# Performance work log

Measured on AMD Instinct MI355X. Metric: run time of the kernel, lower is better.

Reference implementation:

```python
import jax, jax.numpy as jnp
import numpy as np

H, HKV, DH = 16, 8, 128
G = H // HKV
EPS = 1e-6
ROPE_THETA = 1000000.0


def _rms_norm(x, w):
    # RMSNorm over last dim (head_dim)
    var = jnp.mean(x * x, axis=-1, keepdims=True)
    return x * jax.lax.rsqrt(var + EPS) * w


def _rotate_half(x):
    x1, x2 = jnp.split(x, 2, axis=-1)
    return jnp.concatenate([-x2, x1], axis=-1)


def setup_inputs() -> dict:
    key = jax.random.key(0)
    ks = jax.random.split(key, 5)
    B, T, D = 2, 2048, 2048
    s = 0.02
    return {
        "x": jax.random.normal(ks[0], (B, T, D), jnp.float32),
        "wq": jax.random.normal(ks[1], (H * DH, D), jnp.float32) * s,
        "wk": jax.random.normal(ks[2], (HKV * DH, D), jnp.float32) * s,
        "wv": jax.random.normal(ks[3], (HKV * DH, D), jnp.float32) * s,
        "wo": jax.random.normal(ks[4], (D, H * DH), jnp.float32) * s,
        "q_norm_w": jnp.ones((DH,), jnp.float32),
        "k_norm_w": jnp.ones((DH,), jnp.float32),
    }


def reference(x, wq, wk, wv, wo, q_norm_w, k_norm_w):
    B, T, D = x.shape
    # projections (nn.Linear: y = x @ W^T)
    q = (x @ wq.T).reshape(B, T, H, DH).transpose(0, 2, 1, 3)      # [B,H,T,Dh]
    k = (x @ wk.T).reshape(B, T, HKV, DH).transpose(0, 2, 1, 3)    # [B,Hkv,T,Dh]
    v = (x @ wv.T).reshape(B, T, HKV, DH).transpose(0, 2, 1, 3)    # [B,Hkv,T,Dh]

    # QK RMSNorm
    q = _rms_norm(q, q_norm_w)
    k = _rms_norm(k, k_norm_w)

    # RoPE (half-split style), positions 0..T-1
    inv_freq = 1.0 / (ROPE_THETA ** (jnp.arange(0, DH, 2, dtype=jnp.float32) / DH))
    freqs = jnp.arange(T, dtype=jnp.float32)[:, None] * inv_freq[None, :]   # [T,Dh/2]
    emb = jnp.concatenate([freqs, freqs], axis=-1)                           # [T,Dh]
    cos = jnp.cos(emb)[None, None, :, :]
    sin = jnp.sin(emb)[None, None, :, :]
    q = q * cos + _rotate_half(q) * sin
    k = k * cos + _rotate_half(k) * sin

    # GQA attention with fp32 scores and causal mask
    qg = q.reshape(B, HKV, G, T, DH)
    scores = jnp.einsum("bhgtd,bhkd->bhgtk", qg.astype(jnp.float32),
                        k.astype(jnp.float32)) / jnp.sqrt(jnp.float32(DH))
    causal = jnp.tril(jnp.ones((T, T), dtype=bool))[None, None, None, :, :]
    scores = jnp.where(causal, scores, jnp.finfo(jnp.float32).min)
    attn = jax.nn.softmax(scores, axis=-1).astype(x.dtype)
    ctx = jnp.einsum("bhgtk,bhkd->bhgtd", attn, v)                            # [B,Hkv,G,T,Dh]
    out = ctx.reshape(B, H, T, DH).transpose(0, 2, 1, 3).reshape(B, T, H * DH)
    return out @ wo.T
```

## Files before the change

kernel.cpp:

```cpp
#include <hip/hip_runtime.h>
#include <cstdint>

#define Hq 16
#define HKVn 8
#define DHn 128
#define Tn 2048
#define Bn 2
#define Dm 2048
#define BT (Bn*Tn)

typedef __attribute__((ext_vector_type(8))) short bfrag8;
typedef __attribute__((ext_vector_type(4))) float facc4;
typedef __attribute__((ext_vector_type(4))) _Float16 f16x4;
typedef __attribute__((ext_vector_type(8))) _Float16 f16x8;
typedef __attribute__((ext_vector_type(8))) unsigned short us8;

__device__ __forceinline__ unsigned short f2bf(float f) {
    union { float f; unsigned int u; } v; v.f = f;
    unsigned int u = v.u;
    unsigned int r = (u + 0x7FFFu + ((u >> 16) & 1u)) >> 16;
    return (unsigned short)r;
}
__device__ __forceinline__ float bf2f(unsigned short u) {
    union { unsigned int u; float f; } v; v.u = ((unsigned int)u) << 16;
    return v.f;
}

__global__ __launch_bounds__(256) void cvt_all(const float* __restrict__ x,
                                               const float* __restrict__ wq,
                                               const float* __restrict__ wk,
                                               const float* __restrict__ wv,
                                               const float* __restrict__ wo,
                                               unsigned short* __restrict__ x_bf,
                                               unsigned short* __restrict__ wqkv_bf,
                                               unsigned short* __restrict__ wo_bf,
                                               float* __restrict__ lut) {
    int i = blockIdx.x * 256 + threadIdx.x;
    if (i >= 5242880) {
        int ii = i - 5242880;
        int t = ii >> 6, d = ii & 63;
        float fr = exp2f(-(float)d * 0.3114307588956902f);
        float ang = (float)t * fr;
        float sv, cv;
        __sincosf(ang, &sv, &cv);
        lut[t * 128 + d] = cv;
        lut[t * 128 + 64 + d] = sv;
        return;
    }
    const float4* src; ushort4* dst;
    if (i < 2097152)      { src = (const float4*)x  + i;            dst = (ushort4*)x_bf + i; }
    else if (i < 3145728) { src = (const float4*)wq + (i-2097152);  dst = (ushort4*)wqkv_bf + (i-2097152); }
    else if (i < 3670016) { src = (const float4*)wk + (i-3145728);  dst = (ushort4*)wqkv_bf + 1048576 + (i-3145728); }
    else if (i < 4194304) { src = (const float4*)wv + (i-3670016);  dst = (ushort4*)wqkv_bf + 1572864 + (i-3670016); }
    else                  { src = (const float4*)wo + (i-4194304);  dst = (ushort4*)wo_bf + (i-4194304); }
    float4 v = *src;
    ushort4 y;
    y.x = f2bf(v.x); y.y = f2bf(v.y); y.z = f2bf(v.z); y.w = f2bf(v.w);
    *dst = y;
}

__device__ __forceinline__ size_t koff_tiled(int t, int d) {
    int kc = (t >> 4) & 3, l15 = t & 15;
    int f = d >> 5, qd = (d >> 3) & 3, j = d & 7;
    return (size_t)(t >> 6) * 8192 + ((((kc * 4 + f) * 64 + qd * 16 + l15) << 3) + j);
}

__device__ __forceinline__ void stage_half(const unsigned short* __restrict__ g0,
                                           int rowBase, int k0, char* region, int h, int tid) {
#pragma unroll
    for (int s = 0; s < 2; s++) {
        int c = h * 1024 + s * 512 + tid;
        int r = c >> 3;
        int kk = (c & 7) ^ (r & 7);
        const unsigned short* g = g0 + (size_t)(rowBase + r) * 2048 + k0 + kk * 8;
        __builtin_amdgcn_global_load_lds((const __attribute__((address_space(1))) void*)g,
            (__attribute__((address_space(3))) void*)(region + c * 16), 16, 0, 0);
    }
}

__device__ __forceinline__ void stage_half_bt(const unsigned short* __restrict__ g0,
                                              int rowBase, int k0, char* region, int h,
                                              int tid, int K) {
#pragma unroll
    for (int s = 0; s < 2; s++) {
        int c = h * 512 + s * 256 + tid;
        int r = c >> 3;
        int kk = (c & 7) ^ (r & 7);
        const unsigned short* g = g0 + (size_t)(rowBase + r) * K + k0 + kk * 8;
        __builtin_amdgcn_global_load_lds((const __attribute__((address_space(1))) void*)g,
            (__attribute__((address_space(3))) void*)(region + c * 16), 16, 0, 0);
    }
}

__global__ __launch_bounds__(256, 2) void gemm_bt(const unsigned short* __restrict__ A,
                                                  const unsigned short* __restrict__ Bm,
                                                  float* __restrict__ C,
                                                  int M, int N, int K) {
    __shared__ char smem[65536];
    int nt = K >> 6;
    int tid = threadIdx.x;
    int w = tid >> 6, lane = tid & 63, quad = lane >> 4, l15 = lane & 15;
    int wr = w >> 1, wc = w & 1;
    int rowBase = blockIdx.y * 128, colBase = blockIdx.x * 128;
    facc4 acc[4][4];
#pragma unroll
    for (int i = 0; i < 4; i++)
#pragma unroll
        for (int j = 0; j < 4; j++) acc[i][j] = facc4{0.f, 0.f, 0.f, 0.f};

    char* b0A = smem;          char* b0B = smem + 16384;
    char* b1A = smem + 32768;  char* b1B = smem + 49152;
    stage_half_bt(A,  rowBase, 0,  b0A, 0, tid, K);
    stage_half_bt(A,  rowBase, 0,  b0A, 1, tid, K);
    stage_half_bt(Bm, colBase, 0,  b0B, 0, tid, K);
    stage_half_bt(Bm, colBase, 0,  b0B, 1, tid, K);
    stage_half_bt(Bm, colBase, 64, b1B, 0, tid, K);
    stage_half_bt(A,  rowBase, 64, b1A, 0, tid, K);
    stage_half_bt(A,  rowBase, 64, b1A, 1, tid, K);
    asm volatile("s_waitcnt vmcnt(6)" ::: "memory");
    __builtin_amdgcn_s_barrier();

    bfrag8 a01[2][2], a23[2][2], b01[2][2], b23[2][2];
#pragma unroll
    for (int m = 0; m < 2; m++)
#pragma unroll
        for (int kh = 0; kh < 2; kh++) {
            int row = wr * 64 + m * 16 + l15;
            int ch = (kh * 4 + quad) ^ (row & 7);
            a01[m][kh] = *(const bfrag8*)(b0A + row * 128 + ch * 16);
        }
#pragma unroll
    for (int n = 0; n < 2; n++)
#pragma unroll
        for (int kh = 0; kh < 2; kh++) {
            int row = wc * 64 + n * 16 + l15;
            int ch = (kh * 4 + quad) ^ (row & 7);
            b01[n][kh] = *(const bfrag8*)(b0B + row * 128 + ch * 16);
        }

#pragma unroll 1
    for (int t = 0; t < nt; t++) {
        __builtin_amdgcn_sched_barrier(0);
        char* bA = smem + (t & 1) * 32768;
        char* bB = bA + 16384;
        char* oA = smem + ((t & 1) ^ 1) * 32768;
        char* oB = oA + 16384;
        int k1 = (t + 1) * 64, k2 = (t + 2) * 64;

#pragma unroll
        for (int n = 0; n < 2; n++)
#pragma unroll
            for (int kh = 0; kh < 2; kh++) {
                int row = wc * 64 + (2 + n) * 16 + l15;
                int ch = (kh * 4 + quad) ^ (row & 7);
                b23[n][kh] = *(const bfrag8*)(bB + row * 128 + ch * 16);
            }
        if (t + 1 < nt) stage_half_bt(Bm, colBase, k1, oB, 1, tid, K);
        __builtin_amdgcn_sched_barrier(0);
        __builtin_amdgcn_s_barrier();
        __builtin_amdgcn_s_setprio(1);
#pragma unroll
        for (int m = 0; m < 2; m++)
#pragma unroll
            for (int n = 0; n < 2; n++)
#pragma unroll
                for (int kh = 0; kh < 2; kh++)
                    acc[m][n] = __builtin_amdgcn_mfma_f32_16x16x32_bf16(a01[m][kh], b01[n][kh], acc[m][n], 0, 0, 0);
        __builtin_amdgcn_s_setprio(0);
        __builtin_amdgcn_s_barrier();

#pragma unroll
        for (int m = 0; m < 2; m++)
#pragma unroll
            for (int kh = 0; kh < 2; kh++) {
                int row = wr * 64 + (2 + m) * 16 + l15;
                int ch = (kh * 4 + quad) ^ (row & 7);
                a23[m][kh] = *(const bfrag8*)(bA + row * 128 + ch * 16);
            }
        __builtin_amdgcn_sched_barrier(0);
        __builtin_amdgcn_s_barrier();
        __builtin_amdgcn_s_setprio(1);
#pragma unroll
        for (int m = 0; m < 2; m++)
#pragma unroll
            for (int n = 0; n < 2; n++)
#pragma unroll
                for (int kh = 0; kh < 2; kh++)
                    acc[m][2 + n] = __builtin_amdgcn_mfma_f32_16x16x32_bf16(a01[m][kh], b23[n][kh], acc[m][2 + n], 0, 0, 0);
        __builtin_amdgcn_s_setprio(0);
        __builtin_amdgcn_s_barrier();

        if (t + 2 < nt) stage_half_bt(Bm, colBase, k2, bB, 0, tid, K);
        __builtin_amdgcn_sched_barrier(0);
        __builtin_amdgcn_s_barrier();
        __builtin_amdgcn_s_setprio(1);
#pragma unroll
        for (int m = 0; m < 2; m++)
#pragma unroll
            for (int n = 0; n < 2; n++)
#pragma unroll
                for (int kh = 0; kh < 2; kh++)
                    acc[2 + m][2 + n] = __builtin_amdgcn_mfma_f32_16x16x32_bf16(a23[m][kh], b23[n][kh], acc[2 + m][2 + n], 0, 0, 0);
        __builtin_amdgcn_s_setprio(0);
        __builtin_amdgcn_s_barrier();

        if (t + 2 < nt) {
            stage_half_bt(A, rowBase, k2, bA, 0, tid, K);
            stage_half_bt(A, rowBase, k2, bA, 1, tid, K);
            asm volatile("s_waitcnt vmcnt(6)" ::: "memory");
        } else if (t + 1 < nt) {
            asm volatile("s_waitcnt vmcnt(0)" ::: "memory");
        }
        __builtin_amdgcn_sched_barrier(0);
        __builtin_amdgcn_s_barrier();
        __builtin_amdgcn_s_setprio(1);
#pragma unroll
        for (int m = 0; m < 2; m++)
#pragma unroll
            for (int n = 0; n < 2; n++)
#pragma unroll
                for (int kh = 0; kh < 2; kh++)
                    acc[2 + m][n] = __builtin_amdgcn_mfma_f32_16x16x32_bf16(a23[m][kh], b01[n][kh], acc[2 + m][n], 0, 0, 0);
        __builtin_amdgcn_s_setprio(0);
        if (t + 1 < nt) {
#pragma unroll
            for (int m = 0; m < 2; m++)
#pragma unroll
                for (int kh = 0; kh < 2; kh++) {
                    int row = wr * 64 + m * 16 + l15;
                    int ch = (kh * 4 + quad) ^ (row & 7);
                    a01[m][kh] = *(const bfrag8*)(oA + row * 128 + ch * 16);
                }
#pragma unroll
            for (int n = 0; n < 2; n++)
#pragma unroll
                for (int kh = 0; kh < 2; kh++) {
                    int row = wc * 64 + n * 16 + l15;
                    int ch = (kh * 4 + quad) ^ (row & 7);
                    b01[n][kh] = *(const bfrag8*)(oB + row * 128 + ch * 16);
                }
        }
        __builtin_amdgcn_s_barrier();
    }

#pragma unroll
    for (int i = 0; i < 4; i++)
#pragma unroll
        for (int j = 0; j < 4; j++)
#pragma unroll
            for (int r = 0; r < 4; r++) {
                int row = rowBase + wr * 64 + i * 16 + quad * 4 + r;
                int col = colBase + wc * 64 + j * 16 + l15;
                C[(size_t)row * N + col] = acc[i][j][r];
            }
}

__global__ __launch_bounds__(512, 2) void gemm_qkv_fused(const unsigned short* __restrict__ A,
                                                         const unsigned short* __restrict__ Bm,
                                                         const float* __restrict__ qw,
                                                         const float* __restrict__ kw,
                                                         const float* __restrict__ lut,
                                                         unsigned short* __restrict__ q_bf,
                                                         unsigned short* __restrict__ k_bf,
                                                         _Float16* __restrict__ vT) {
    __shared__ char smem[131072];
    const int NT = 32;
    int tid = threadIdx.x;
    int w = tid >> 6, lane = tid & 63, quad = lane >> 4, l15 = lane & 15;
    int wr = w >> 2, wc = w & 3;
    int u = ((blockIdx.x & 7) << 5) | (blockIdx.x >> 3);
    int bx = u & 15, by = u >> 4;
    int rowBase = by * 256, colBase = bx * 256;

    facc4 acc[8][4];
#pragma unroll
    for (int m = 0; m < 8; m++)
#pragma unroll
        for (int n = 0; n < 4; n++) acc[m][n] = facc4{0.f, 0.f, 0.f, 0.f};

    char* b0A = smem;           char* b0B = smem + 32768;
    char* b1A = smem + 65536;   char* b1B = smem + 98304;
    stage_half(A,  rowBase, 0,  b0A, 0, tid);
    stage_half(A,  rowBase, 0,  b0A, 1, tid);
    stage_half(Bm, colBase, 0,  b0B, 0, tid);
    stage_half(Bm, colBase, 0,  b0B, 1, tid);
    stage_half(Bm, colBase, 64, b1B, 0, tid);
    stage_half(A,  rowBase, 64, b1A, 0, tid);
    stage_half(A,  rowBase, 64, b1A, 1, tid);
    asm volatile("s_waitcnt vmcnt(6)" ::: "memory");
    __builtin_amdgcn_s_barrier();

    bfrag8 a03[4][2], a47[4][2], b01[2][2], b23[2][2];
#pragma unroll
    for (int m = 0; m < 4; m++)
#pragma unroll
        for (int kh = 0; kh < 2; kh++) {
            int row = wr * 128 + m * 16 + l15;
            int ch = (kh * 4 + quad) ^ (row & 7);
            a03[m][kh] = *(const bfrag8*)(b0A + row * 128 + ch * 16);
        }
#pragma unroll
    for (int n = 0; n < 2; n++)
#pragma unroll
        for (int kh = 0; kh < 2; kh++) {
            int row = wc * 64 + n * 16 + l15;
            int ch = (kh * 4 + quad) ^ (row & 7);
            b01[n][kh] = *(const bfrag8*)(b0B + row * 128 + ch * 16);
        }

#pragma unroll 1
    for (int t = 0; t < NT; t++) {
        __builtin_amdgcn_sched_barrier(0);
        char* bA = smem + (t & 1) * 65536;
        char* bB = bA + 32768;
        char* oA = smem + ((t & 1) ^ 1) * 65536;
        char* oB = oA + 32768;
        int k1 = (t + 1) * 64, k2 = (t + 2) * 64;

#pragma unroll
        for (int n = 0; n < 2; n++)
#pragma unroll
            for (int kh = 0; kh < 2; kh++) {
                int row = wc * 64 + (2 + n) * 16 + l15;
                int ch = (kh * 4 + quad) ^ (row & 7);
                b23[n][kh] = *(const bfrag8*)(bB + row * 128 + ch * 16);
            }
        if (t + 1 < NT) stage_half(Bm, colBase, k1, oB, 1, tid);
        __builtin_amdgcn_sched_barrier(0);
        __builtin_amdgcn_s_barrier();
        __builtin_amdgcn_s_setprio(1);
#pragma unroll
        for (int m = 0; m < 4; m++)
#pragma unroll
            for (int n = 0; n < 2; n++)
#pragma unroll
                for (int kh = 0; kh < 2; kh++)
                    acc[m][n] = __builtin_amdgcn_mfma_f32_16x16x32_bf16(a03[m][kh], b01[n][kh], acc[m][n], 0, 0, 0);
        __builtin_amdgcn_s_setprio(0);
        __builtin_amdgcn_s_barrier();

#pragma unroll
        for (int m = 0; m < 4; m++)
#pragma unroll
            for (int kh = 0; kh < 2; kh++) {
                int row = wr * 128 + (4 + m) * 16 + l15;
                int ch = (kh * 4 + quad) ^ (row & 7);
                a47[m][kh] = *(const bfrag8*)(bA + row * 128 + ch * 16);
            }
        __builtin_amdgcn_sched_barrier(0);
        __builtin_amdgcn_s_barrier();
        __builtin_amdgcn_s_setprio(1);
#pragma unroll
        for (int m = 0; m < 4; m++)
#pragma unroll
            for (int n = 0; n < 2; n++)
#pragma unroll
                for (int kh = 0; kh < 2; kh++)
                    acc[m][2 + n] = __builtin_amdgcn_mfma_f32_16x16x32_bf16(a03[m][kh], b23[n][kh], acc[m][2 + n], 0, 0, 0);
        __builtin_amdgcn_s_setprio(0);
        __builtin_amdgcn_s_barrier();

        if (t + 2 < NT) stage_half(Bm, colBase, k2, bB, 0, tid);
        __builtin_amdgcn_sched_barrier(0);
        __builtin_amdgcn_s_barrier();
        __builtin_amdgcn_s_setprio(1);
#pragma unroll
        for (int m = 0; m < 4; m++)
#pragma unroll
            for (int n = 0; n < 2; n++)
#pragma unroll
                for (int kh = 0; kh < 2; kh++)
                    acc[4 + m][2 + n] = __builtin_amdgcn_mfma_f32_16x16x32_bf16(a47[m][kh], b23[n][kh], acc[4 + m][2 + n], 0, 0, 0);
        __builtin_amdgcn_s_setprio(0);
        __builtin_amdgcn_s_barrier();

        if (t + 2 < NT) {
            stage_half(A, rowBase, k2, bA, 0, tid);
            stage_half(A, rowBase, k2, bA, 1, tid);
            asm volatile("s_waitcnt vmcnt(6)" ::: "memory");
        } else if (t + 1 < NT) {
            asm volatile("s_waitcnt vmcnt(0)" ::: "memory");
        }
        __builtin_amdgcn_sched_barrier(0);
        __builtin_amdgcn_s_barrier();
        __builtin_amdgcn_s_setprio(1);
#pragma unroll
        for (int m = 0; m < 4; m++)
#pragma unroll
            for (int n = 0; n < 2; n++)
#pragma unroll
                for (int kh = 0; kh < 2; kh++)
                    acc[4 + m][n] = __builtin_amdgcn_mfma_f32_16x16x32_bf16(a47[m][kh], b01[n][kh], acc[4 + m][n], 0, 0, 0);
        __builtin_amdgcn_s_setprio(0);
        if (t + 1 < NT) {
#pragma unroll
            for (int m = 0; m < 4; m++)
#pragma unroll
                for (int kh = 0; kh < 2; kh++) {
                    int row = wr * 128 + m * 16 + l15;
                    int ch = (kh * 4 + quad) ^ (row & 7);
                    a03[m][kh] = *(const bfrag8*)(oA + row * 128 + ch * 16);
                }
#pragma unroll
            for (int n = 0; n < 2; n++)
#pragma unroll
                for (int kh = 0; kh < 2; kh++) {
                    int row = wc * 64 + n * 16 + l15;
                    int ch = (kh * 4 + quad) ^ (row & 7);
                    b01[n][kh] = *(const bfrag8*)(oB + row * 128 + ch * 16);
                }
        }
        __builtin_amdgcn_s_barrier();
    }

    if (bx >= 12) {
        int hv = (bx - 12) * 2 + (wc >> 1);
#pragma unroll
        for (int half = 0; half < 2; half++) {
            int gt0 = rowBase + wr * 128 + half * 64;
            int bb = gt0 >> 11, t64 = (gt0 & 2047) >> 6;
            _Float16* vbase = vT + ((size_t)(bb * 8 + hv) * 32 + t64) * 8192;
#pragma unroll
            for (int mm = 0; mm < 4; mm++) {
                int kcp = mm >> 1, hh = mm & 1;
#pragma unroll
                for (int n = 0; n < 4; n++) {
                    int dblk = (wc & 1) * 4 + n;
                    f16x4 pv;
#pragma unroll
                    for (int r = 0; r < 4; r++) pv[r] = (_Float16)acc[half * 4 + mm][n][r];
                    *(f16x4*)(vbase + (((dblk * 2 + kcp) * 64 + quad * 16 + l15) * 8) + hh * 4) = pv;
                }
            }
        }
        return;
    }

    const float* wn = (bx < 8) ? qw : kw;
    const float osc = (bx < 8) ? (0.08838834764831845f * 1.4426950408889634f) : 1.0f;
    float* sums = (float*)smem;
#pragma unroll
    for (int m = 0; m < 8; m++)
#pragma unroll
        for (int r = 0; r < 4; r++) {
            float s = 0.f;
#pragma unroll
            for (int n = 0; n < 4; n++) s += acc[m][n][r] * acc[m][n][r];
            s += __shfl_xor(s, 1); s += __shfl_xor(s, 2);
            s += __shfl_xor(s, 4); s += __shfl_xor(s, 8);
            if (l15 == 0) sums[wc * 256 + wr * 128 + m * 16 + quad * 4 + r] = s;
        }
    __syncthreads();
    int hw = wc >> 1;
    float inv[8][4];
#pragma unroll
    for (int m = 0; m < 8; m++)
#pragma unroll
        for (int r = 0; r < 4; r++) {
            int row = wr * 128 + m * 16 + quad * 4 + r;
            float tot = sums[(2 * hw) * 256 + row] + sums[(2 * hw + 1) * 256 + row];
            inv[m][r] = rsqrtf(tot * (1.0f / 128.0f) + 1e-6f);
        }
    __syncthreads();
    unsigned short* tileb = (unsigned short*)(smem + hw * 65536);
    float wcol[4];
#pragma unroll
    for (int n = 0; n < 4; n++) wcol[n] = wn[(wc & 1) * 64 + n * 16 + l15];
#pragma unroll
    for (int m = 0; m < 8; m++)
#pragma unroll
        for (int r = 0; r < 4; r++) {
            int row = wr * 128 + m * 16 + quad * 4 + r;
            int sw = (row & 7) << 4;
#pragma unroll
            for (int n = 0; n < 4; n++) {
                int cb = ((wc & 1) * 64 + n * 16 + l15) * 2;
                *(unsigned short*)((char*)tileb + row * 256 + (cb ^ sw)) =
                    f2bf(acc[m][n][r] * inv[m][r] * wcol[n]);
            }
        }
    __syncthreads();
    {
        int row = tid >> 1, d0 = (tid & 1) * 32;
        int gt = rowBase + row;
        int tt = gt & 2047, bb = gt >> 11;
        const float* lc = lut + tt * 128;
        int sw = (row & 7) << 4;
#pragma unroll
        for (int hh2 = 0; hh2 < 2; hh2++) {
            const char* tb = (const char*)(smem + hh2 * 65536);
            unsigned short* qrow = 0; unsigned short* kplane = 0;
            if (bx < 8) qrow = q_bf + ((size_t)(bb * 16 + bx * 2 + hh2) * 2048 + tt) * 128;
            else        kplane = k_bf + (size_t)(bb * 8 + (bx - 8) * 2 + hh2) * 2048 * 128;
#pragma unroll
            for (int dc = 0; dc < 32; dc += 8) {
                int db = d0 + dc;
                us8 n0u = *(const us8*)(tb + row * 256 + ((2 * db) ^ sw));
                us8 n1u = *(const us8*)(tb + row * 256 + ((2 * db + 128) ^ sw));
                float4 cA = *(const float4*)(lc + db), cB = *(const float4*)(lc + db + 4);
                float4 sA = *(const float4*)(lc + 64 + db), sB = *(const float4*)(lc + 64 + db + 4);
                float cv[8] = {cA.x, cA.y, cA.z, cA.w, cB.x, cB.y, cB.z, cB.w};
                float sv[8] = {sA.x, sA.y, sA.z, sA.w, sB.x, sB.y, sB.z, sB.w};
                us8 p0, p1;
#pragma unroll
                for (int e = 0; e < 8; e++) {
                    float a0 = bf2f(n0u[e]), a1 = bf2f(n1u[e]);
                    p0[e] = f2bf((a0 * cv[e] - a1 * sv[e]) * osc);
                    p1[e] = f2bf((a1 * cv[e] + a0 * sv[e]) * osc);
                }
                if (bx < 8) {
                    *(us8*)(qrow + db) = p0;
                    *(us8*)(qrow + db + 64) = p1;
                } else {
                    *(us8*)(kplane + koff_tiled(tt, db)) = p0;
                    *(us8*)(kplane + koff_tiled(tt, db + 64)) = p1;
                }
            }
        }
    }
}

__global__ __launch_bounds__(256, 2) void attn_kernel(const unsigned short* __restrict__ q_bf,
                                                      const unsigned short* __restrict__ k_glob,
                                                      const _Float16* __restrict__ v_glob,
                                                      unsigned short* __restrict__ ctx) {
    __shared__ char smem[65536];
    int tid = threadIdx.x;
    int w = tid >> 6, lane = tid & 63, quad = lane >> 4, l15 = lane & 15;
    int bid = blockIdx.x;
    int u = bid & 255, halfg = bid >> 8;
    int j = u & 7, h = (u >> 3) & 15, b = (u >> 7) & 1;
    int qblk = halfg ? j : 15 - j;
    int hkv = h >> 1;
    int qb = qblk * 128;
    int qw0 = qb + w * 32;

    const unsigned short* qp = q_bf + (size_t)(b * Hq + h) * Tn * 128;
    const unsigned short* ktile = k_glob + (size_t)(b * HKVn + hkv) * 32 * 8192;
    const _Float16* vtile = v_glob + (size_t)(b * HKVn + hkv) * 32 * 8192;

    bfrag8 qf[2][4];
#pragma unroll
    for (int g = 0; g < 2; g++) {
        int row = qw0 + g * 16 + l15;
#pragma unroll
        for (int f = 0; f < 4; f++)
            qf[g][f] = *(const bfrag8*)(qp + (size_t)row * 128 + f * 32 + quad * 8);
    }

    facc4 o0[8], o1[8];
#pragma unroll
    for (int jj = 0; jj < 8; jj++) { o0[jj] = facc4{0.f,0.f,0.f,0.f}; o1[jj] = facc4{0.f,0.f,0.f,0.f}; }
    float m0 = -__builtin_inff(), m1 = -__builtin_inff(), l0 = 0.f, l1 = 0.f;

    int nkb = qb / 64 + 2;
#pragma unroll
    for (int i = 0; i < 4; i++) {
        const unsigned short* gk = ktile + (size_t)(i * 256 + tid) * 8;
        __builtin_amdgcn_global_load_lds((const __attribute__((address_space(1))) void*)gk,
            (__attribute__((address_space(3))) void*)(smem + i * 4096 + w * 1024), 16, 0, 0);
        const _Float16* gv = vtile + (size_t)(i * 256 + tid) * 8;
        __builtin_amdgcn_global_load_lds((const __attribute__((address_space(1))) void*)gv,
            (__attribute__((address_space(3))) void*)(smem + 16384 + i * 4096 + w * 1024), 16, 0, 0);
    }

    for (int ib = 0; ib < nkb; ib++) {
        int kb = ib * 64;
        __syncthreads();
        if (ib + 1 < nkb) {
            char* nb = smem + ((ib + 1) & 1) * 32768;
#pragma unroll
            for (int i = 0; i < 4; i++) {
                const unsigned short* gk = ktile + (size_t)(ib + 1) * 8192 + (i * 256 + tid) * 8;
                __builtin_amdgcn_global_load_lds((const __attribute__((address_space(1))) void*)gk,
                    (__attribute__((address_space(3))) void*)(nb + i * 4096 + w * 1024), 16, 0, 0);
                const _Float16* gv = vtile + (size_t)(ib + 1) * 8192 + (i * 256 + tid) * 8;
                __builtin_amdgcn_global_load_lds((const __attribute__((address_space(1))) void*)gv,
                    (__attribute__((address_space(3))) void*)(nb + 16384 + i * 4096 + w * 1024), 16, 0, 0);
            }
        }
        char* cb = smem + (ib & 1) * 32768;
        if (kb <= qw0 + 31) {
            facc4 s0[4], s1[4];
#pragma unroll
            for (int kc = 0; kc < 4; kc++) {
                bfrag8 kf[4];
#pragma unroll
                for (int f = 0; f < 4; f++)
                    kf[f] = *(const bfrag8*)(cb + (((kc * 4 + f) * 64 + lane) << 4));
                facc4 a = facc4{0.f,0.f,0.f,0.f}, bq = facc4{0.f,0.f,0.f,0.f};
#pragma unroll
                for (int f = 0; f < 4; f++) {
                    a  = __builtin_amdgcn_mfma_f32_16x16x32_bf16(kf[f], qf[0][f], a, 0, 0, 0);
                    bq = __builtin_amdgcn_mfma_f32_16x16x32_bf16(kf[f], qf[1][f], bq, 0, 0, 0);
                }
                s0[kc] = a; s1[kc] = bq;
            }
            if (kb + 63 > qw0) {
                int q0 = qw0 + l15, q1 = q0 + 16;
#pragma unroll
                for (int kc = 0; kc < 4; kc++)
#pragma unroll
                    for (int r = 0; r < 4; r++) {
                        int k = kb + kc * 16 + quad * 4 + r;
                        if (k > q0) s0[kc][r] = -__builtin_inff();
                        if (k > q1) s1[kc][r] = -__builtin_inff();
                    }
            }
            float mx0 = s0[0][0], mx1 = s1[0][0];
#pragma unroll
            for (int kc = 0; kc < 4; kc++)
#pragma unroll
                for (int r = 0; r < 4; r++) {
                    mx0 = fmaxf(mx0, s0[kc][r]); mx1 = fmaxf(mx1, s1[kc][r]);
                }
            mx0 = fmaxf(mx0, __shfl_xor(mx0, 16)); mx0 = fmaxf(mx0, __shfl_xor(mx0, 32));
            mx1 = fmaxf(mx1, __shfl_xor(mx1, 16)); mx1 = fmaxf(mx1, __shfl_xor(mx1, 32));
            if (!__all((mx0 - m0 <= 8.f) && (mx1 - m1 <= 8.f))) {
                float mn0 = fmaxf(m0, mx0), mn1 = fmaxf(m1, mx1);
                float alpha0 = exp2f(m0 - mn0), alpha1 = exp2f(m1 - mn1);
                m0 = mn0; m1 = mn1;
                l0 *= alpha0; l1 *= alpha1;
#pragma unroll
                for (int jj = 0; jj < 8; jj++)
#pragma unroll
                    for (int r = 0; r < 4; r++) { o0[jj][r] *= alpha0; o1[jj][r] *= alpha1; }
            }
            float rs0 = 0.f, rs1 = 0.f;
#pragma unroll
            for (int kc = 0; kc < 4; kc++)
#pragma unroll
                for (int r = 0; r < 4; r++) {
                    s0[kc][r] = exp2f(s0[kc][r] - m0); rs0 += s0[kc][r];
                    s1[kc][r] = exp2f(s1[kc][r] - m1); rs1 += s1[kc][r];
                }
            rs0 += __shfl_xor(rs0, 16); rs0 += __shfl_xor(rs0, 32);
            rs1 += __shfl_xor(rs1, 16); rs1 += __shfl_xor(rs1, 32);
            l0 += rs0; l1 += rs1;
            f16x4 pb0[4], pb1[4];
#pragma unroll
            for (int kc = 0; kc < 4; kc++) {
                pb0[kc] = f16x4{(_Float16)s0[kc][0], (_Float16)s0[kc][1],
                                (_Float16)s0[kc][2], (_Float16)s0[kc][3]};
                pb1[kc] = f16x4{(_Float16)s1[kc][0], (_Float16)s1[kc][1],
                                (_Float16)s1[kc][2], (_Float16)s1[kc][3]};
            }
#pragma unroll
            for (int kcp = 0; kcp < 2; kcp++)
#pragma unroll
                for (int dblk = 0; dblk < 8; dblk++) {
                    f16x8 vv = *(const f16x8*)(cb + 16384 + (((dblk * 2 + kcp) * 64 + lane) << 4));
                    f16x4 a0 = f16x4{vv[0], vv[1], vv[2], vv[3]};
                    f16x4 a1 = f16x4{vv[4], vv[5], vv[6], vv[7]};
                    o0[dblk] = __builtin_amdgcn_mfma_f32_16x16x16f16(a0, pb0[kcp*2],   o0[dblk], 0, 0, 0);
                    o0[dblk] = __builtin_amdgcn_mfma_f32_16x16x16f16(a1, pb0[kcp*2+1], o0[dblk], 0, 0, 0);
                    o1[dblk] = __builtin_amdgcn_mfma_f32_16x16x16f16(a0, pb1[kcp*2],   o1[dblk], 0, 0, 0);
                    o1[dblk] = __builtin_amdgcn_mfma_f32_16x16x16f16(a1, pb1[kcp*2+1], o1[dblk], 0, 0, 0);
                }
        }
    }
    float inv0 = 1.0f / l0, inv1 = 1.0f / l1;
#pragma unroll
    for (int g = 0; g < 2; g++) {
        int q = qw0 + g * 16 + l15;
        float invl = g ? inv1 : inv0;
#pragma unroll
        for (int dblk = 0; dblk < 8; dblk++) {
            facc4 ov = g ? o1[dblk] : o0[dblk];
            ushort4 st;
            st.x = f2bf(ov[0] * invl); st.y = f2bf(ov[1] * invl);
            st.z = f2bf(ov[2] * invl); st.w = f2bf(ov[3] * invl);
            *(ushort4*)(ctx + ((size_t)(b * Tn + q)) * 2048 + h * 128 + dblk * 16 + quad * 4) = st;
        }
    }
}

extern "C" void kernel_launch(void* const* d_in, const int* in_sizes, int n_in,
                              void* d_out, int out_size, void* d_ws, size_t ws_size,
                              hipStream_t stream) {
    (void)in_sizes; (void)n_in; (void)out_size; (void)ws_size;
    const float* x  = (const float*)d_in[0];
    const float* wq = (const float*)d_in[1];
    const float* wk = (const float*)d_in[2];
    const float* wv = (const float*)d_in[3];
    const float* wo = (const float*)d_in[4];
    const float* qw = (const float*)d_in[5];
    const float* kw = (const float*)d_in[6];
    float* out = (float*)d_out;
    char* ws = (char*)d_ws;

    unsigned short* x_bf    = (unsigned short*)(ws);
    unsigned short* wqkv_bf = (unsigned short*)(ws + 16777216);
    unsigned short* wo_bf   = (unsigned short*)(ws + 33554432);
    unsigned short* q_bf    = (unsigned short*)(ws + 41943040);
    unsigned short* k_bf    = (unsigned short*)(ws + 58720256);
    _Float16*       vT_f16  = (_Float16*)(ws + 67108864);
    unsigned short* ctx_bf  = (unsigned short*)(ws + 75497472);
    float*          lut     = (float*)(ws + 92274688);

    cvt_all<<<20992, 256, 0, stream>>>(x, wq, wk, wv, wo, x_bf, wqkv_bf, wo_bf, lut);
    gemm_qkv_fused<<<256, 512, 0, stream>>>(x_bf, wqkv_bf, qw, kw, lut, q_bf, k_bf, vT_f16);
    attn_kernel<<<512, 256, 0, stream>>>(q_bf, k_bf, vT_f16, ctx_bf);
    gemm_bt<<<dim3(16, 32), 256, 0, stream>>>(ctx_bf, wo_bf, out, 4096, 2048, 2048);
}
```

Measured before the change: 313.0 us.

## Shrink attention query tile to 64 rows and read V directly from global

The attention kernel now gives each block 64 query rows (16 per wave) instead of 128, doubling the grid to 1024 blocks and raising the occupancy hint to 4 blocks per CU. V tiles are no longer staged in LDS; each wave reads its V fragments straight from global memory, so LDS use halves and only K is double-buffered. This aims for more parallelism and better causal load balance. The cost is that K/V reuse per block falls and V traffic goes through uncached-in-LDS global loads on the critical path.

```diff
diff --git a/kernel.cpp b/kernel.cpp
--- a/kernel.cpp
+++ b/kernel.cpp
@@ -520,158 +520,134 @@
     }
 }
 
-__global__ __launch_bounds__(256, 2) void attn_kernel(const unsigned short* __restrict__ q_bf,
+__global__ __launch_bounds__(256, 4) void attn_kernel(const unsigned short* __restrict__ q_bf,
                                                       const unsigned short* __restrict__ k_glob,
                                                       const _Float16* __restrict__ v_glob,
                                                       unsigned short* __restrict__ ctx) {
-    __shared__ char smem[65536];
+    __shared__ char smem[32768];
     int tid = threadIdx.x;
     int w = tid >> 6, lane = tid & 63, quad = lane >> 4, l15 = lane & 15;
     int bid = blockIdx.x;
-    int u = bid & 255, halfg = bid >> 8;
-    int j = u & 7, h = (u >> 3) & 15, b = (u >> 7) & 1;
-    int qblk = halfg ? j : 15 - j;
+    int u = bid & 511, halfg = bid >> 9;
+    int j = u & 15, h = (u >> 4) & 15, b = (u >> 8) & 1;
+    int qblk = halfg ? j : 31 - j;
     int hkv = h >> 1;
-    int qb = qblk * 128;
-    int qw0 = qb + w * 32;
+    int qb = qblk * 64;
+    int qw0 = qb + w * 16;
 
     const unsigned short* qp = q_bf + (size_t)(b * Hq + h) * Tn * 128;
     const unsigned short* ktile = k_glob + (size_t)(b * HKVn + hkv) * 32 * 8192;
     const _Float16* vtile = v_glob + (size_t)(b * HKVn + hkv) * 32 * 8192;
 
-    bfrag8 qf[2][4];
-#pragma unroll
-    for (int g = 0; g < 2; g++) {
-        int row = qw0 + g * 16 + l15;
+    bfrag8 qf[4];
+    {
+        int row = qw0 + l15;
 #pragma unroll
         for (int f = 0; f < 4; f++)
-            qf[g][f] = *(const bfrag8*)(qp + (size_t)row * 128 + f * 32 + quad * 8);
-    }
-
-    facc4 o0[8], o1[8];
-#pragma unroll
-    for (int jj = 0; jj < 8; jj++) { o0[jj] = facc4{0.f,0.f,0.f,0.f}; o1[jj] = facc4{0.f,0.f,0.f,0.f}; }
-    float m0 = -__builtin_inff(), m1 = -__builtin_inff(), l0 = 0.f, l1 = 0.f;
-
-    int nkb = qb / 64 + 2;
+            qf[f] = *(const bfrag8*)(qp + (size_t)row * 128 + f * 32 + quad * 8);
+    }
+
+    facc4 o[8];
+#pragma unroll
+    for (int d = 0; d < 8; d++) o[d] = facc4{0.f, 0.f, 0.f, 0.f};
+    float m0 = -__builtin_inff(), l0 = 0.f;
+
+    int nkb = qblk + 1;
 #pragma unroll
     for (int i = 0; i < 4; i++) {
         const unsigned short* gk = ktile + (size_t)(i * 256 + tid) * 8;
         __builtin_amdgcn_global_load_lds((const __attribute__((address_space(1))) void*)gk,
             (__attribute__((address_space(3))) void*)(smem + i * 4096 + w * 1024), 16, 0, 0);
-        const _Float16* gv = vtile + (size_t)(i * 256 + tid) * 8;
-        __builtin_amdgcn_global_load_lds((const __attribute__((address_space(1))) void*)gv,
-            (__attribute__((address_space(3))) void*)(smem + 16384 + i * 4096 + w * 1024), 16, 0, 0);
     }
 
     for (int ib = 0; ib < nkb; ib++) {
         int kb = ib * 64;
         __syncthreads();
         if (ib + 1 < nkb) {
-            char* nb = smem + ((ib + 1) & 1) * 32768;
+            char* nb = smem + ((ib + 1) & 1) * 16384;
 #pragma unroll
             for (int i = 0; i < 4; i++) {
                 const unsigned short* gk = ktile + (size_t)(ib + 1) * 8192 + (i * 256 + tid) * 8;
                 __builtin_amdgcn_global_load_lds((const __attribute__((address_space(1))) void*)gk,
                     (__attribute__((address_space(3))) void*)(nb + i * 4096 + w * 1024), 16, 0, 0);
-                const _Float16* gv = vtile + (size_t)(ib + 1) * 8192 + (i * 256 + tid) * 8;
-                __builtin_amdgcn_global_load_lds((const __attribute__((address_space(1))) void*)gv,
-                    (__attribute__((address_space(3))) void*)(nb + 16384 + i * 4096 + w * 1024), 16, 0, 0);
-            }
-        }
-        char* cb = smem + (ib & 1) * 32768;
-        if (kb <= qw0 + 31) {
-            facc4 s0[4], s1[4];
+            }
+        }
+        char* cb = smem + (ib & 1) * 16384;
+        if (kb <= qw0 + 15) {
+            facc4 s0[4];
 #pragma unroll
             for (int kc = 0; kc < 4; kc++) {
                 bfrag8 kf[4];
 #pragma unroll
                 for (int f = 0; f < 4; f++)
                     kf[f] = *(const bfrag8*)(cb + (((kc * 4 + f) * 64 + lane) << 4));
-                facc4 a = facc4{0.f,0.f,0.f,0.f}, bq = facc4{0.f,0.f,0.f,0.f};
-#pragma unroll
-                for (int f = 0; f < 4; f++) {
-                    a  = __builtin_amdgcn_mfma_f32_16x16x32_bf16(kf[f], qf[0][f], a, 0, 0, 0);
-                    bq = __builtin_amdgcn_mfma_f32_16x16x32_bf16(kf[f], qf[1][f], bq, 0, 0, 0);
-                }
-                s0[kc] = a; s1[kc] = bq;
+                facc4 a = facc4{0.f, 0.f, 0.f, 0.f};
+#pragma unroll
+                for (int f = 0; f < 4; f++)
+                    a = __builtin_amdgcn_mfma_f32_16x16x32_bf16(kf[f], qf[f], a, 0, 0, 0);
+                s0[kc] = a;
             }
             if (kb + 63 > qw0) {
-                int q0 = qw0 + l15, q1 = q0 + 16;
+                int q0 = qw0 + l15;
 #pragma unroll
                 for (int kc = 0; kc < 4; kc++)
 #pragma unroll
                     for (int r = 0; r < 4; r++) {
                         int k = kb + kc * 16 + quad * 4 + r;
                         if (k > q0) s0[kc][r] = -__builtin_inff();
-                        if (k > q1) s1[kc][r] = -__builtin_inff();
                     }
             }
-            float mx0 = s0[0][0], mx1 = s1[0][0];
+            float mx0 = s0[0][0];
 #pragma unroll
             for (int kc = 0; kc < 4; kc++)
 #pragma unroll
-                for (int r = 0; r < 4; r++) {
-                    mx0 = fmaxf(mx0, s0[kc][r]); mx1 = fmaxf(mx1, s1[kc][r]);
-                }
+                for (int r = 0; r < 4; r++) mx0 = fmaxf(mx0, s0[kc][r]);
             mx0 = fmaxf(mx0, __shfl_xor(mx0, 16)); mx0 = fmaxf(mx0, __shfl_xor(mx0, 32));
-            mx1 = fmaxf(mx1, __shfl_xor(mx1, 16)); mx1 = fmaxf(mx1, __shfl_xor(mx1, 32));
-            if (!__all((mx0 - m0 <= 8.f) && (mx1 - m1 <= 8.f))) {
-                float mn0 = fmaxf(m0, mx0), mn1 = fmaxf(m1, mx1);
-                float alpha0 = exp2f(m0 - mn0), alpha1 = exp2f(m1 - mn1);
-                m0 = mn0; m1 = mn1;
-                l0 *= alpha0; l1 *= alpha1;
-#pragma unroll
-                for (int jj = 0; jj < 8; jj++)
-#pragma unroll
-                    for (int r = 0; r < 4; r++) { o0[jj][r] *= alpha0; o1[jj][r] *= alpha1; }
-            }
-            float rs0 = 0.f, rs1 = 0.f;
+            if (!__all(mx0 - m0 <= 8.f)) {
+                float mn0 = fmaxf(m0, mx0);
+                float alpha0 = exp2f(m0 - mn0);
+                m0 = mn0;
+                l0 *= alpha0;
+#pragma unroll
+                for (int d = 0; d < 8; d++)
+#pragma unroll
+                    for (int r = 0; r < 4; r++) o[d][r] *= alpha0;
+            }
+            float rs0 = 0.f;
 #pragma unroll
             for (int kc = 0; kc < 4; kc++)
 #pragma unroll
                 for (int r = 0; r < 4; r++) {
                     s0[kc][r] = exp2f(s0[kc][r] - m0); rs0 += s0[kc][r];
-                    s1[kc][r] = exp2f(s1[kc][r] - m1); rs1 += s1[kc][r];
                 }
             rs0 += __shfl_xor(rs0, 16); rs0 += __shfl_xor(rs0, 32);
-            rs1 += __shfl_xor(rs1, 16); rs1 += __shfl_xor(rs1, 32);
-            l0 += rs0; l1 += rs1;
-            f16x4 pb0[4], pb1[4];
-#pragma unroll
-            for (int kc = 0; kc < 4; kc++) {
-                pb0[kc] = f16x4{(_Float16)s0[kc][0], (_Float16)s0[kc][1],
-                                (_Float16)s0[kc][2], (_Float16)s0[kc][3]};
-                pb1[kc] = f16x4{(_Float16)s1[kc][0], (_Float16)s1[kc][1],
-                                (_Float16)s1[kc][2], (_Float16)s1[kc][3]};
-            }
+            l0 += rs0;
+            f16x4 pb[4];
+#pragma unroll
+            for (int kc = 0; kc < 4; kc++)
+                pb[kc] = f16x4{(_Float16)s0[kc][0], (_Float16)s0[kc][1],
+                               (_Float16)s0[kc][2], (_Float16)s0[kc][3]};
+            const _Float16* vb = vtile + (size_t)ib * 8192;
 #pragma unroll
             for (int kcp = 0; kcp < 2; kcp++)
 #pragma unroll
                 for (int dblk = 0; dblk < 8; dblk++) {
-                    f16x8 vv = *(const f16x8*)(cb + 16384 + (((dblk * 2 + kcp) * 64 + lane) << 4));
+                    f16x8 vv = *(const f16x8*)(vb + (((dblk * 2 + kcp) * 64 + lane) << 3));
                     f16x4 a0 = f16x4{vv[0], vv[1], vv[2], vv[3]};
                     f16x4 a1 = f16x4{vv[4], vv[5], vv[6], vv[7]};
-                    o0[dblk] = __builtin_amdgcn_mfma_f32_16x16x16f16(a0, pb0[kcp*2],   o0[dblk], 0, 0, 0);
-                    o0[dblk] = __builtin_amdgcn_mfma_f32_16x16x16f16(a1, pb0[kcp*2+1], o0[dblk], 0, 0, 0);
-                    o1[dblk] = __builtin_amdgcn_mfma_f32_16x16x16f16(a0, pb1[kcp*2],   o1[dblk], 0, 0, 0);
-                    o1[dblk] = __builtin_amdgcn_mfma_f32_16x16x16f16(a1, pb1[kcp*2+1], o1[dblk], 0, 0, 0);
-                }
-        }
-    }
-    float inv0 = 1.0f / l0, inv1 = 1.0f / l1;
-#pragma unroll
-    for (int g = 0; g < 2; g++) {
-        int q = qw0 + g * 16 + l15;
-        float invl = g ? inv1 : inv0;
-#pragma unroll
-        for (int dblk = 0; dblk < 8; dblk++) {
-            facc4 ov = g ? o1[dblk] : o0[dblk];
-            ushort4 st;
-            st.x = f2bf(ov[0] * invl); st.y = f2bf(ov[1] * invl);
-            st.z = f2bf(ov[2] * invl); st.w = f2bf(ov[3] * invl);
-            *(ushort4*)(ctx + ((size_t)(b * Tn + q)) * 2048 + h * 128 + dblk * 16 + quad * 4) = st;
-        }
+                    o[dblk] = __builtin_amdgcn_mfma_f32_16x16x16f16(a0, pb[kcp * 2],     o[dblk], 0, 0, 0);
+                    o[dblk] = __builtin_amdgcn_mfma_f32_16x16x16f16(a1, pb[kcp * 2 + 1], o[dblk], 0, 0, 0);
+                }
+        }
+    }
+    float inv0 = 1.0f / l0;
+    int q = qw0 + l15;
+#pragma unroll
+    for (int dblk = 0; dblk < 8; dblk++) {
+        ushort4 st;
+        st.x = f2bf(o[dblk][0] * inv0); st.y = f2bf(o[dblk][1] * inv0);
+        st.z = f2bf(o[dblk][2] * inv0); st.w = f2bf(o[dblk][3] * inv0);
+        *(ushort4*)(ctx + ((size_t)(b * Tn + q)) * 2048 + h * 128 + dblk * 16 + quad * 4) = st;
     }
 }
 
@@ -700,6 +676,6 @@
 
     cvt_all<<<20992, 256, 0, stream>>>(x, wq, wk, wv, wo, x_bf, wqkv_bf, wo_bf, lut);
     gemm_qkv_fused<<<256, 512, 0, stream>>>(x_bf, wqkv_bf, qw, kw, lut, q_bf, k_bf, vT_f16);
-    attn_kernel<<<512, 256, 0, stream>>>(q_bf, k_bf, vT_f16, ctx_bf);
+    attn_kernel<<<1024, 256, 0, stream>>>(q_bf, k_bf, vT_f16, ctx_bf);
     gemm_bt<<<dim3(16, 32), 256, 0, stream>>>(ctx_bf, wo_bf, out, 4096, 2048, 2048);
 }
```

After: 350.3 us. +11.9%, slower.
